# Optimization experiments

Measured on AMD Instinct MI355X. Metric: run time of the kernel, lower is better.

The kernel has to match this reference:

```python
import jax, jax.numpy as jnp
import numpy as np

K_F = 3          # propagation kernel
PAD_F = 1
NUM = K_F * K_F - 1   # 8 non-reference neighbors
IDX_REF = NUM // 2    # 4
PROP_TIME = 18
B, H, W = 4, 240, 1216


def _conv2d_same(x, w, b):
    # x: (B,Cin,H,W), w: (Cout,Cin,kh,kw)
    y = jax.lax.conv_general_dilated(x, w, (1, 1), 'SAME',
                                     dimension_numbers=('NCHW', 'OIHW', 'NCHW'))
    return y + b[None, :, None, None]


def _bilinear(img, y, x):
    # img: (B,H,W); y,x: (B,K,H,W) float sample coords. Zero outside bounds (DCN semantics).
    Bv, Hv, Wv = img.shape
    flat = img.reshape(Bv, -1)
    y0 = jnp.floor(y)
    x0 = jnp.floor(x)
    wy = y - y0
    wx = x - x0

    def g(yy, xx):
        valid = (yy >= 0) & (yy <= Hv - 1) & (xx >= 0) & (xx <= Wv - 1)
        yc = jnp.clip(yy, 0, Hv - 1).astype(jnp.int32)
        xc = jnp.clip(xx, 0, Wv - 1).astype(jnp.int32)
        idx = (yc * Wv + xc).reshape(Bv, -1)
        v = jnp.take_along_axis(flat, idx, axis=1).reshape(yy.shape)
        return jnp.where(valid, v, jnp.zeros((), img.dtype))

    return ((1 - wy) * (1 - wx) * g(y0, x0)
            + (1 - wy) * wx * g(y0, x0 + 1)
            + wy * (1 - wx) * g(y1 := y0 + 1, x0)
            + wy * wx * g(y1, x0 + 1))


def _deform_agg(feat, off, mask, k, pad):
    # Modulated deformable conv with w == 1, b == 0, ch_f == 1.
    # feat: (B,1,H,W); off: (B,K,2,H,W) (dy,dx); mask: (B,K,H,W)
    Bv, _, Hv, Wv = feat.shape
    kk = jnp.arange(k)
    by = (jnp.repeat(kk, k) - pad).astype(feat.dtype)  # kernel base dy, row-major
    bx = (jnp.tile(kk, k) - pad).astype(feat.dtype)    # kernel base dx
    gy = jnp.arange(Hv, dtype=feat.dtype)[None, None, :, None]
    gx = jnp.arange(Wv, dtype=feat.dtype)[None, None, None, :]
    y = gy + by[None, :, None, None] + off[:, :, 0]
    x = gx + bx[None, :, None, None] + off[:, :, 1]
    s = _bilinear(feat[:, 0], y, x)                    # (B,K,H,W)
    return jnp.sum(s * mask, axis=1, keepdims=True)


def setup_inputs() -> dict:
    key = jax.random.key(0)
    k1, k2, k3, k4, k5, k6 = jax.random.split(key, 6)
    feat_init = jax.random.uniform(k1, (B, 1, H, W), jnp.float32)
    guidance = jax.random.normal(k2, (B, 8, H, W), jnp.float32)
    confidence = jax.random.uniform(k3, (B, 1, H, W), jnp.float32)
    dep = jax.random.uniform(k4, (B, 1, H, W), jnp.float32)
    valid = (jax.random.uniform(k5, (B, 1, H, W), jnp.float32) < 0.05)
    feat_fix = dep * valid.astype(jnp.float32)
    w_oa = 0.1 * jax.random.normal(k6, (3 * NUM, 8, 3, 3), jnp.float32)
    b_oa = jnp.zeros((3 * NUM,), jnp.float32)
    aff_scale_const = jnp.full((1,), 0.5 * NUM, jnp.float32)  # gamma * num (TGASS)
    return {'feat_init': feat_init, 'guidance': guidance, 'confidence': confidence,
            'feat_fix': feat_fix, 'w_oa': w_oa, 'b_oa': b_oa,
            'aff_scale_const': aff_scale_const}


def reference(feat_init, guidance, confidence, feat_fix, w_oa, b_oa, aff_scale_const):
    Bv, _, Hv, Wv = guidance.shape
    oa = _conv2d_same(guidance, w_oa, b_oa)                 # (B,24,H,W)
    o1, o2, aff = oa[:, :NUM], oa[:, NUM:2 * NUM], oa[:, 2 * NUM:]
    # torch: cat((o1,o2),1).view(B,num,2,H,W) then insert zero ref offset at idx_ref
    off = jnp.concatenate([o1, o2], axis=1).reshape(Bv, NUM, 2, Hv, Wv)
    zeros = jnp.zeros((Bv, 1, 2, Hv, Wv), off.dtype)
    off = jnp.concatenate([off[:, :IDX_REF], zeros, off[:, IDX_REF:]], axis=1)  # (B,9,2,H,W)

    # TGASS affinity
    aff = jnp.tanh(aff) / (aff_scale_const + 1e-8)          # (B,8,H,W)

    # confidence-weighted affinity: 1x1 deform-sample of confidence at each neighbor offset
    nbr = jnp.array([0, 1, 2, 3, 5, 6, 7, 8])
    off_c = jax.lax.stop_gradient(off[:, nbr])              # (B,8,2,H,W), offsets detached
    gy = jnp.arange(Hv, dtype=aff.dtype)[None, None, :, None]
    gx = jnp.arange(Wv, dtype=aff.dtype)[None, None, None, :]
    conf_aff = _bilinear(confidence[:, 0], gy + off_c[:, :, 0], gx + off_c[:, :, 1])
    aff = aff * conf_aff

    s = jnp.sum(jnp.abs(aff), axis=1, keepdims=True) + 1e-4
    s = jnp.maximum(s, 1.0)                                 # TGASS clamp
    aff = aff / s
    aff_ref = 1.0 - jnp.sum(aff, axis=1, keepdims=True)
    aff9 = jnp.concatenate([aff[:, :IDX_REF], aff_ref, aff[:, IDX_REF:]], axis=1)  # (B,9,H,W)

    # preserve_input mask
    mask_fix = (jnp.sum((feat_fix > 0.0).astype(feat_fix.dtype), axis=1, keepdims=True) > 0.0)
    mask_fix = jax.lax.stop_gradient(mask_fix.astype(feat_fix.dtype))

    def step(feat, _):
        feat = (1.0 - mask_fix) * feat + mask_fix * feat_fix
        feat = _deform_agg(feat, off, aff9, K_F, PAD_F)
        return feat, None

    feat_result, _ = jax.lax.scan(step, feat_init, None, length=PROP_TIME)
    return feat_result, off.reshape(Bv, -1, Hv, Wv), aff9
```

## Files before the change

### kernel.cpp

```cpp
#include <hip/hip_runtime.h>
#include <hip/hip_bf16.h>

#define B_ 4
#define H_ 240
#define W_ 1216
#define HW_ (H_*W_)
#define N1_ (B_*HW_)
#define PT_ 18

#define PR_ 4
#define TROWS2 (PR_ + 10)
#define TCOLS 274

__device__ __forceinline__ bool probe_bf16(const void* scale_ptr) {
    return ((const unsigned short*)scale_ptr)[0] == 0x4080;
}

__device__ __forceinline__ float ldin(const void* p, int i, bool bf) {
    if (bf) {
        unsigned int u = (unsigned int)((const unsigned short*)p)[i];
        return __uint_as_float(u << 16);
    }
    return ((const float*)p)[i];
}

__device__ __forceinline__ void stout(void* p, int i, bool bf, float v) {
    if (bf) ((__hip_bfloat16*)p)[i] = __float2bfloat16(v);
    else    ((float*)p)[i] = v;
}

__global__ __launch_bounds__(256) void k_prep_w(const void* __restrict__ w_oa,
                                                const void* __restrict__ b_oa,
                                                const void* __restrict__ scale,
                                                float* __restrict__ wc) {
    bool bf = probe_bf16(scale);
    int i = blockIdx.x * 256 + threadIdx.x;
    if (i < 1728) wc[i] = ldin(w_oa, i, bf);
    if (i < 24)   wc[1728 + i] = ldin(b_oa, i, bf);
}

__global__ __launch_bounds__(256) void k_init(const void* __restrict__ finit,
                                              const void* __restrict__ ffix,
                                              const void* __restrict__ scale,
                                              float* __restrict__ featA) {
    bool bf = probe_bf16(scale);
    int p = blockIdx.x * 256 + threadIdx.x;
    if (p >= N1_) return;
    float fx = ldin(ffix, p, bf);
    featA[p] = (fx > 0.0f) ? fx : ldin(finit, p, bf);
}

__global__ __launch_bounds__(256) void k_conv(const void* __restrict__ guid,
                                              const void* __restrict__ conf,
                                              const void* __restrict__ scale,
                                              const float* __restrict__ wc,
                                              void* __restrict__ d_out,
                                              float* __restrict__ ws_off,
                                              float* __restrict__ ws_aff,
                                              int mode2) {
    bool bf = probe_bf16(scale);
    int p = blockIdx.x * 256 + threadIdx.x;
    if (p >= N1_) return;
    int b = p / HW_;
    int r = p - b * HW_;
    int h = r / W_;
    int w = r - h * W_;

    float g[8][9];
    #pragma unroll
    for (int t = 0; t < 9; ++t) {
        int hh = h + t / 3 - 1;
        int ww = w + t % 3 - 1;
        bool v = (hh >= 0) && (hh < H_) && (ww >= 0) && (ww < W_);
        int idx0 = hh * W_ + ww;
        #pragma unroll
        for (int ci = 0; ci < 8; ++ci)
            g[ci][t] = v ? ldin(guid, (b * 8 + ci) * HW_ + idx0, bf) : 0.0f;
    }

    float oa[24];
    #pragma unroll
    for (int co = 0; co < 24; ++co) {
        float a = wc[1728 + co];
        #pragma unroll
        for (int ci = 0; ci < 8; ++ci)
            #pragma unroll
            for (int t = 0; t < 9; ++t)
                a = fmaf(g[ci][t], wc[(co * 8 + ci) * 9 + t], a);
        oa[co] = a;
    }

    float scl = ldin(scale, 0, bf);
    float inv = 1.0f / (scl + 1e-8f);

    float aft[8];
    int cbase = b * HW_;
    #pragma unroll
    for (int t = 0; t < 8; ++t) {
        float a = tanhf(oa[16 + t]) * inv;
        float y = (float)h + oa[2 * t];
        float x = (float)w + oa[2 * t + 1];
        float y0f = floorf(y), x0f = floorf(x);
        int y0 = (int)y0f, x0 = (int)x0f;
        float wy = y - y0f, wx = x - x0f;
        int y0c = min(max(y0, 0), H_ - 1), y1c = min(max(y0 + 1, 0), H_ - 1);
        int x0c = min(max(x0, 0), W_ - 1), x1c = min(max(x0 + 1, 0), W_ - 1);
        bool vy0 = (y0 >= 0) && (y0 < H_), vy1 = (y0 >= -1) && (y0 < H_ - 1);
        bool vx0 = (x0 >= 0) && (x0 < W_), vx1 = (x0 >= -1) && (x0 < W_ - 1);
        float w00 = (1.0f - wy) * (1.0f - wx); w00 = (vy0 && vx0) ? w00 : 0.0f;
        float w01 = (1.0f - wy) * wx;          w01 = (vy0 && vx1) ? w01 : 0.0f;
        float w10 = wy * (1.0f - wx);          w10 = (vy1 && vx0) ? w10 : 0.0f;
        float w11 = wy * wx;                   w11 = (vy1 && vx1) ? w11 : 0.0f;
        float f00 = ldin(conf, cbase + y0c * W_ + x0c, bf);
        float f01 = ldin(conf, cbase + y0c * W_ + x1c, bf);
        float f10 = ldin(conf, cbase + y1c * W_ + x0c, bf);
        float f11 = ldin(conf, cbase + y1c * W_ + x1c, bf);
        float cv = w00 * f00 + w01 * f01 + w10 * f10 + w11 * f11;
        aft[t] = a * cv;
    }
    float s = 1e-4f;
    #pragma unroll
    for (int t = 0; t < 8; ++t) s += fabsf(aft[t]);
    s = fmaxf(s, 1.0f);
    float rs = 1.0f / s;
    float suma = 0.0f;
    #pragma unroll
    for (int t = 0; t < 8; ++t) { aft[t] *= rs; suma += aft[t]; }
    float aref = 1.0f - suma;

    #pragma unroll
    for (int t = 0; t < 8; ++t) {
        int n9 = t + (t >= 4 ? 1 : 0);
        stout(d_out, N1_ + (b * 18 + 2 * n9)     * HW_ + r, bf, oa[2 * t]);
        stout(d_out, N1_ + (b * 18 + 2 * n9 + 1) * HW_ + r, bf, oa[2 * t + 1]);
        stout(d_out, 19 * N1_ + (b * 9 + n9) * HW_ + r, bf, aft[t]);
    }
    stout(d_out, N1_ + (b * 18 + 8) * HW_ + r, bf, 0.0f);
    stout(d_out, N1_ + (b * 18 + 9) * HW_ + r, bf, 0.0f);
    stout(d_out, 19 * N1_ + (b * 9 + 4) * HW_ + r, bf, aref);

    if (mode2 && bf) {
        #pragma unroll
        for (int t = 0; t < 8; ++t) {
            ws_off[t * N1_ + p]       = oa[2 * t];
            ws_off[(8 + t) * N1_ + p] = oa[2 * t + 1];
            int n9 = t + (t >= 4 ? 1 : 0);
            ws_aff[n9 * N1_ + p] = aft[t];
        }
        ws_aff[4 * N1_ + p] = aref;
    }
}

__global__ __launch_bounds__(256) void k_prop(const float* __restrict__ src,
                                              float* __restrict__ dst,
                                              const float* __restrict__ ws_off,
                                              const float* __restrict__ ws_aff,
                                              const void* __restrict__ d_out_all,
                                              const void* __restrict__ ffix_in,
                                              const void* __restrict__ scale,
                                              void* __restrict__ d_out_feat,
                                              int last, int mode2) {
    __shared__ float tile[TROWS2][TCOLS];

    int tx = threadIdx.x;
    int bx = blockIdx.x;
    int h0 = blockIdx.y * PR_;
    int b  = blockIdx.z;
    int w  = bx * 256 + tx;
    bool active = (w < W_);
    bool bf = probe_bf16(scale);
    bool use_ws = (mode2 != 0) && bf;

    const float* sp = src + b * HW_;
    int row0 = h0 - 5;
    int col0 = bx * 256 - 8;

    for (int idx = tx; idx < TROWS2 * TCOLS; idx += 256) {
        int rr = idx / TCOLS;
        int cc = idx - rr * TCOLS;
        int gy = min(max(row0 + rr, 0), H_ - 1);
        int gx = min(max(col0 + cc, 0), W_ - 1);
        tile[rr][cc] = sp[gy * W_ + gx];
    }
    __syncthreads();
    if (!active) return;

    for (int ry = 0; ry < PR_; ++ry) {
        int h = h0 + ry;
        int r = h * W_ + w;
        int p = b * HW_ + r;

        float oy[8], ox[8], af[9];
        if (use_ws) {
            #pragma unroll
            for (int t = 0; t < 8; ++t) {
                oy[t] = ws_off[t * N1_ + p];
                ox[t] = ws_off[(8 + t) * N1_ + p];
            }
            #pragma unroll
            for (int n = 0; n < 9; ++n) af[n] = ws_aff[n * N1_ + p];
        } else {
            #pragma unroll
            for (int t = 0; t < 8; ++t) {
                int n9 = t + (t >= 4 ? 1 : 0);
                oy[t] = ldin(d_out_all, N1_ + (b * 18 + 2 * n9)     * HW_ + r, bf);
                ox[t] = ldin(d_out_all, N1_ + (b * 18 + 2 * n9 + 1) * HW_ + r, bf);
            }
            #pragma unroll
            for (int n = 0; n < 9; ++n)
                af[n] = ldin(d_out_all, 19 * N1_ + (b * 9 + n) * HW_ + r, bf);
        }

        float acc = af[4] * tile[5 + ry][tx + 8];

        #pragma unroll
        for (int t = 0; t < 8; ++t) {
            int n9 = t + (t >= 4 ? 1 : 0);
            float y = (float)(h + n9 / 3 - 1) + oy[t];
            float x = (float)(w + n9 % 3 - 1) + ox[t];
            float y0f = floorf(y), x0f = floorf(x);
            int y0 = (int)y0f, x0 = (int)x0f;
            float wy = y - y0f, wx = x - x0f;
            int y0c = min(max(y0, 0), H_ - 1), y1c = min(max(y0 + 1, 0), H_ - 1);
            int x0c = min(max(x0, 0), W_ - 1), x1c = min(max(x0 + 1, 0), W_ - 1);
            bool vy0 = (y0 >= 0) && (y0 < H_), vy1 = (y0 >= -1) && (y0 < H_ - 1);
            bool vx0 = (x0 >= 0) && (x0 < W_), vx1 = (x0 >= -1) && (x0 < W_ - 1);
            float w00 = (1.0f - wy) * (1.0f - wx); w00 = (vy0 && vx0) ? w00 : 0.0f;
            float w01 = (1.0f - wy) * wx;          w01 = (vy0 && vx1) ? w01 : 0.0f;
            float w10 = wy * (1.0f - wx);          w10 = (vy1 && vx0) ? w10 : 0.0f;
            float w11 = wy * wx;                   w11 = (vy1 && vx1) ? w11 : 0.0f;

            int sy0 = y0c - row0, sy1 = y1c - row0;
            int sx0 = x0c - col0, sx1 = x1c - col0;
            float f00, f01, f10, f11;
            if ((sy0 >= 0) && (sy1 <= TROWS2 - 1) && (sx0 >= 0) && (sx1 <= TCOLS - 1)) {
                f00 = tile[sy0][sx0];
                f01 = tile[sy0][sx1];
                f10 = tile[sy1][sx0];
                f11 = tile[sy1][sx1];
            } else {
                f00 = sp[y0c * W_ + x0c];
                f01 = sp[y0c * W_ + x1c];
                f10 = sp[y1c * W_ + x0c];
                f11 = sp[y1c * W_ + x1c];
            }
            float v = w00 * f00 + w01 * f01 + w10 * f10 + w11 * f11;
            acc = fmaf(af[n9], v, acc);
        }

        if (last) {
            stout(d_out_feat, p, bf, acc);
        } else {
            float fxv = ldin(ffix_in, p, bf);
            dst[p] = (fxv > 0.0f) ? fxv : acc;
        }
    }
}

extern "C" void kernel_launch(void* const* d_in, const int* in_sizes, int n_in,
                              void* d_out, int out_size, void* d_ws, size_t ws_size,
                              hipStream_t stream) {
    const void* feat_init  = d_in[0];
    const void* guidance   = d_in[1];
    const void* confidence = d_in[2];
    const void* feat_fix   = d_in[3];
    const void* w_oa       = d_in[4];
    const void* b_oa       = d_in[5];
    const void* scale      = d_in[6];

    float* wsf    = (float*)d_ws;
    float* featA  = wsf;
    float* featB  = wsf + N1_;
    float* wc     = wsf + 2 * (size_t)N1_;
    float* ws_off = wsf + 2 * (size_t)N1_ + 4096;
    float* ws_aff = ws_off + 16 * (size_t)N1_;

    size_t need2 = ((size_t)27 * N1_ + 4096) * sizeof(float);
    int mode2 = (ws_size >= need2) ? 1 : 0;

    int grid = (N1_ + 255) / 256;
    hipLaunchKernelGGL(k_prep_w, dim3(7), dim3(256), 0, stream, w_oa, b_oa, scale, wc);
    hipLaunchKernelGGL(k_init, dim3(grid), dim3(256), 0, stream,
                       feat_init, feat_fix, scale, featA);
    hipLaunchKernelGGL(k_conv, dim3(grid), dim3(256), 0, stream,
                       guidance, confidence, scale, wc, d_out, ws_off, ws_aff, mode2);

    float* a = featA;
    float* bbuf = featB;
    dim3 pgrid(5, H_ / PR_, B_);
    for (int it = 0; it < PT_; ++it) {
        int last = (it == PT_ - 1) ? 1 : 0;
        hipLaunchKernelGGL(k_prop, pgrid, dim3(256), 0, stream,
                           a, bbuf, ws_off, ws_aff, d_out, feat_fix, scale,
                           d_out, last, mode2);
        float* t = a; a = bbuf; bbuf = t;
    }
}
```

Baseline: 990.5 us.

## Replace per-step fixed-depth reload with bitmask, template dtype paths, restructure conv loop

The init kernel now builds a 64-bit ballot bitmask of fixed (sparse-depth) pixels and writes the initial feature into both ping-pong buffers. Each propagation step then skips storing fixed pixels instead of reloading feat_fix every iteration, which cuts global reads in the 18 prop launches. Kernels are templated on bf16/fp32 so the dtype branch is resolved once per launch. The conv loop is reordered to load one input channel at a time, which lowers register pressure. Correctness relies on fixed pixels already holding their value in both buffers, and the grid size now assumes N1 is divisible by 256.

```diff
diff --git a/kernel.cpp b/kernel.cpp
--- a/kernel.cpp
+++ b/kernel.cpp
@@ -16,16 +16,18 @@
     return ((const unsigned short*)scale_ptr)[0] == 0x4080;
 }
 
-__device__ __forceinline__ float ldin(const void* p, int i, bool bf) {
-    if (bf) {
+template<bool BF>
+__device__ __forceinline__ float ldT(const void* p, int i) {
+    if (BF) {
         unsigned int u = (unsigned int)((const unsigned short*)p)[i];
         return __uint_as_float(u << 16);
     }
     return ((const float*)p)[i];
 }
 
-__device__ __forceinline__ void stout(void* p, int i, bool bf, float v) {
-    if (bf) ((__hip_bfloat16*)p)[i] = __float2bfloat16(v);
+template<bool BF>
+__device__ __forceinline__ void stT(void* p, int i, float v) {
+    if (BF) ((__hip_bfloat16*)p)[i] = __float2bfloat16(v);
     else    ((float*)p)[i] = v;
 }
 
@@ -35,62 +37,71 @@
                                                 float* __restrict__ wc) {
     bool bf = probe_bf16(scale);
     int i = blockIdx.x * 256 + threadIdx.x;
-    if (i < 1728) wc[i] = ldin(w_oa, i, bf);
-    if (i < 24)   wc[1728 + i] = ldin(b_oa, i, bf);
+    if (i < 1728) wc[i] = bf ? ldT<true>(w_oa, i) : ldT<false>(w_oa, i);
+    if (i < 24)   wc[1728 + i] = bf ? ldT<true>(b_oa, i) : ldT<false>(b_oa, i);
 }
 
 __global__ __launch_bounds__(256) void k_init(const void* __restrict__ finit,
                                               const void* __restrict__ ffix,
                                               const void* __restrict__ scale,
-                                              float* __restrict__ featA) {
+                                              float* __restrict__ featA,
+                                              float* __restrict__ featB,
+                                              unsigned long long* __restrict__ mask64) {
     bool bf = probe_bf16(scale);
     int p = blockIdx.x * 256 + threadIdx.x;
-    if (p >= N1_) return;
-    float fx = ldin(ffix, p, bf);
-    featA[p] = (fx > 0.0f) ? fx : ldin(finit, p, bf);
-}
-
-__global__ __launch_bounds__(256) void k_conv(const void* __restrict__ guid,
-                                              const void* __restrict__ conf,
-                                              const void* __restrict__ scale,
-                                              const float* __restrict__ wc,
-                                              void* __restrict__ d_out,
-                                              float* __restrict__ ws_off,
-                                              float* __restrict__ ws_aff,
-                                              int mode2) {
-    bool bf = probe_bf16(scale);
+    float fx = bf ? ldT<true>(ffix, p)  : ldT<false>(ffix, p);
+    float fi = bf ? ldT<true>(finit, p) : ldT<false>(finit, p);
+    bool fixed = fx > 0.0f;
+    float v = fixed ? fx : fi;
+    featA[p] = v;
+    featB[p] = v;
+    unsigned long long bal = __ballot(fixed);
+    if ((threadIdx.x & 63) == 0) mask64[p >> 6] = bal;
+}
+
+template<bool BF>
+__device__ __forceinline__ void conv_body(const void* __restrict__ guid,
+                                          const void* __restrict__ conf,
+                                          const void* __restrict__ scale,
+                                          const float* __restrict__ wc,
+                                          void* __restrict__ d_out,
+                                          float* __restrict__ ws_off,
+                                          float* __restrict__ ws_aff,
+                                          int mode2) {
     int p = blockIdx.x * 256 + threadIdx.x;
-    if (p >= N1_) return;
     int b = p / HW_;
     int r = p - b * HW_;
     int h = r / W_;
     int w = r - h * W_;
 
-    float g[8][9];
+    int idx0[9]; bool vld[9];
     #pragma unroll
     for (int t = 0; t < 9; ++t) {
         int hh = h + t / 3 - 1;
         int ww = w + t % 3 - 1;
-        bool v = (hh >= 0) && (hh < H_) && (ww >= 0) && (ww < W_);
-        int idx0 = hh * W_ + ww;
+        vld[t] = (hh >= 0) && (hh < H_) && (ww >= 0) && (ww < W_);
+        idx0[t] = hh * W_ + ww;
+    }
+
+    float oa[24];
+    #pragma unroll
+    for (int co = 0; co < 24; ++co) oa[co] = wc[1728 + co];
+
+    #pragma unroll
+    for (int ci = 0; ci < 8; ++ci) {
+        int cb = (b * 8 + ci) * HW_;
+        float gv[9];
         #pragma unroll
-        for (int ci = 0; ci < 8; ++ci)
-            g[ci][t] = v ? ldin(guid, (b * 8 + ci) * HW_ + idx0, bf) : 0.0f;
-    }
-
-    float oa[24];
-    #pragma unroll
-    for (int co = 0; co < 24; ++co) {
-        float a = wc[1728 + co];
+        for (int t = 0; t < 9; ++t)
+            gv[t] = vld[t] ? ldT<BF>(guid, cb + idx0[t]) : 0.0f;
         #pragma unroll
-        for (int ci = 0; ci < 8; ++ci)
+        for (int co = 0; co < 24; ++co)
             #pragma unroll
             for (int t = 0; t < 9; ++t)
-                a = fmaf(g[ci][t], wc[(co * 8 + ci) * 9 + t], a);
-        oa[co] = a;
-    }
-
-    float scl = ldin(scale, 0, bf);
+                oa[co] = fmaf(gv[t], wc[(co * 8 + ci) * 9 + t], oa[co]);
+    }
+
+    float scl = ldT<BF>(scale, 0);
     float inv = 1.0f / (scl + 1e-8f);
 
     float aft[8];
@@ -111,10 +122,10 @@
         float w01 = (1.0f - wy) * wx;          w01 = (vy0 && vx1) ? w01 : 0.0f;
         float w10 = wy * (1.0f - wx);          w10 = (vy1 && vx0) ? w10 : 0.0f;
         float w11 = wy * wx;                   w11 = (vy1 && vx1) ? w11 : 0.0f;
-        float f00 = ldin(conf, cbase + y0c * W_ + x0c, bf);
-        float f01 = ldin(conf, cbase + y0c * W_ + x1c, bf);
-        float f10 = ldin(conf, cbase + y1c * W_ + x0c, bf);
-        float f11 = ldin(conf, cbase + y1c * W_ + x1c, bf);
+        float f00 = ldT<BF>(conf, cbase + y0c * W_ + x0c);
+        float f01 = ldT<BF>(conf, cbase + y0c * W_ + x1c);
+        float f10 = ldT<BF>(conf, cbase + y1c * W_ + x0c);
+        float f11 = ldT<BF>(conf, cbase + y1c * W_ + x1c);
         float cv = w00 * f00 + w01 * f01 + w10 * f10 + w11 * f11;
         aft[t] = a * cv;
     }
@@ -131,15 +142,15 @@
     #pragma unroll
     for (int t = 0; t < 8; ++t) {
         int n9 = t + (t >= 4 ? 1 : 0);
-        stout(d_out, N1_ + (b * 18 + 2 * n9)     * HW_ + r, bf, oa[2 * t]);
-        stout(d_out, N1_ + (b * 18 + 2 * n9 + 1) * HW_ + r, bf, oa[2 * t + 1]);
-        stout(d_out, 19 * N1_ + (b * 9 + n9) * HW_ + r, bf, aft[t]);
-    }
-    stout(d_out, N1_ + (b * 18 + 8) * HW_ + r, bf, 0.0f);
-    stout(d_out, N1_ + (b * 18 + 9) * HW_ + r, bf, 0.0f);
-    stout(d_out, 19 * N1_ + (b * 9 + 4) * HW_ + r, bf, aref);
-
-    if (mode2 && bf) {
+        stT<BF>(d_out, N1_ + (b * 18 + 2 * n9)     * HW_ + r, oa[2 * t]);
+        stT<BF>(d_out, N1_ + (b * 18 + 2 * n9 + 1) * HW_ + r, oa[2 * t + 1]);
+        stT<BF>(d_out, 19 * N1_ + (b * 9 + n9) * HW_ + r, aft[t]);
+    }
+    stT<BF>(d_out, N1_ + (b * 18 + 8) * HW_ + r, 0.0f);
+    stT<BF>(d_out, N1_ + (b * 18 + 9) * HW_ + r, 0.0f);
+    stT<BF>(d_out, 19 * N1_ + (b * 9 + 4) * HW_ + r, aref);
+
+    if (BF && mode2) {
         #pragma unroll
         for (int t = 0; t < 8; ++t) {
             ws_off[t * N1_ + p]       = oa[2 * t];
@@ -151,25 +162,37 @@
     }
 }
 
-__global__ __launch_bounds__(256) void k_prop(const float* __restrict__ src,
-                                              float* __restrict__ dst,
-                                              const float* __restrict__ ws_off,
-                                              const float* __restrict__ ws_aff,
-                                              const void* __restrict__ d_out_all,
-                                              const void* __restrict__ ffix_in,
+__global__ __launch_bounds__(256) void k_conv(const void* __restrict__ guid,
+                                              const void* __restrict__ conf,
                                               const void* __restrict__ scale,
-                                              void* __restrict__ d_out_feat,
-                                              int last, int mode2) {
-    __shared__ float tile[TROWS2][TCOLS];
-
+                                              const float* __restrict__ wc,
+                                              void* __restrict__ d_out,
+                                              float* __restrict__ ws_off,
+                                              float* __restrict__ ws_aff,
+                                              int mode2) {
+    if (probe_bf16(scale))
+        conv_body<true>(guid, conf, scale, wc, d_out, ws_off, ws_aff, mode2);
+    else
+        conv_body<false>(guid, conf, scale, wc, d_out, ws_off, ws_aff, mode2);
+}
+
+template<bool BF>
+__device__ __forceinline__ void prop_body(float (*tile)[TCOLS],
+                                          const float* __restrict__ src,
+                                          float* __restrict__ dst,
+                                          const float* __restrict__ ws_off,
+                                          const float* __restrict__ ws_aff,
+                                          const void* __restrict__ d_out_all,
+                                          const unsigned long long* __restrict__ mask64,
+                                          void* __restrict__ d_out_feat,
+                                          int last, int mode2) {
     int tx = threadIdx.x;
     int bx = blockIdx.x;
     int h0 = blockIdx.y * PR_;
     int b  = blockIdx.z;
     int w  = bx * 256 + tx;
     bool active = (w < W_);
-    bool bf = probe_bf16(scale);
-    bool use_ws = (mode2 != 0) && bf;
+    bool use_ws = BF && (mode2 != 0);
 
     const float* sp = src + b * HW_;
     int row0 = h0 - 5;
@@ -203,12 +226,12 @@
             #pragma unroll
             for (int t = 0; t < 8; ++t) {
                 int n9 = t + (t >= 4 ? 1 : 0);
-                oy[t] = ldin(d_out_all, N1_ + (b * 18 + 2 * n9)     * HW_ + r, bf);
-                ox[t] = ldin(d_out_all, N1_ + (b * 18 + 2 * n9 + 1) * HW_ + r, bf);
+                oy[t] = ldT<BF>(d_out_all, N1_ + (b * 18 + 2 * n9)     * HW_ + r);
+                ox[t] = ldT<BF>(d_out_all, N1_ + (b * 18 + 2 * n9 + 1) * HW_ + r);
             }
             #pragma unroll
             for (int n = 0; n < 9; ++n)
-                af[n] = ldin(d_out_all, 19 * N1_ + (b * 9 + n) * HW_ + r, bf);
+                af[n] = ldT<BF>(d_out_all, 19 * N1_ + (b * 9 + n) * HW_ + r);
         }
 
         float acc = af[4] * tile[5 + ry][tx + 8];
@@ -249,12 +272,31 @@
         }
 
         if (last) {
-            stout(d_out_feat, p, bf, acc);
+            stT<BF>(d_out_feat, p, acc);
         } else {
-            float fxv = ldin(ffix_in, p, bf);
-            dst[p] = (fxv > 0.0f) ? fxv : acc;
+            unsigned long long bal = mask64[p >> 6];
+            bool fixed = (bal >> (p & 63)) & 1ull;
+            if (!fixed) dst[p] = acc;
         }
     }
+}
+
+__global__ __launch_bounds__(256) void k_prop(const float* __restrict__ src,
+                                              float* __restrict__ dst,
+                                              const float* __restrict__ ws_off,
+                                              const float* __restrict__ ws_aff,
+                                              const void* __restrict__ d_out_all,
+                                              const unsigned long long* __restrict__ mask64,
+                                              const void* __restrict__ scale,
+                                              void* __restrict__ d_out_feat,
+                                              int last, int mode2) {
+    __shared__ float tile[TROWS2][TCOLS];
+    if (probe_bf16(scale))
+        prop_body<true>(tile, src, dst, ws_off, ws_aff, d_out_all, mask64,
+                        d_out_feat, last, mode2);
+    else
+        prop_body<false>(tile, src, dst, ws_off, ws_aff, d_out_all, mask64,
+                         d_out_feat, last, mode2);
 }
 
 extern "C" void kernel_launch(void* const* d_in, const int* in_sizes, int n_in,
@@ -272,16 +314,18 @@
     float* featA  = wsf;
     float* featB  = wsf + N1_;
     float* wc     = wsf + 2 * (size_t)N1_;
-    float* ws_off = wsf + 2 * (size_t)N1_ + 4096;
+    unsigned long long* mask64 =
+        (unsigned long long*)(wsf + 2 * (size_t)N1_ + 2048);
+    float* ws_off = wsf + 2 * (size_t)N1_ + 2048 + 36480;
     float* ws_aff = ws_off + 16 * (size_t)N1_;
 
-    size_t need2 = ((size_t)27 * N1_ + 4096) * sizeof(float);
+    size_t need2 = ((size_t)27 * N1_ + 2048 + 36480) * sizeof(float);
     int mode2 = (ws_size >= need2) ? 1 : 0;
 
-    int grid = (N1_ + 255) / 256;
+    int grid = N1_ / 256;
     hipLaunchKernelGGL(k_prep_w, dim3(7), dim3(256), 0, stream, w_oa, b_oa, scale, wc);
     hipLaunchKernelGGL(k_init, dim3(grid), dim3(256), 0, stream,
-                       feat_init, feat_fix, scale, featA);
+                       feat_init, feat_fix, scale, featA, featB, mask64);
     hipLaunchKernelGGL(k_conv, dim3(grid), dim3(256), 0, stream,
                        guidance, confidence, scale, wc, d_out, ws_off, ws_aff, mode2);
 
@@ -291,7 +335,7 @@
     for (int it = 0; it < PT_; ++it) {
         int last = (it == PT_ - 1) ? 1 : 0;
         hipLaunchKernelGGL(k_prop, pgrid, dim3(256), 0, stream,
-                           a, bbuf, ws_off, ws_aff, d_out, feat_fix, scale,
+                           a, bbuf, ws_off, ws_aff, d_out, mask64, scale,
                            d_out, last, mode2);
         float* t = a; a = bbuf; bbuf = t;
     }
```

After: 987.8 us. About the same (-0.3%).

## Precompute fixed-pixel bitmask, skip fixed writes, template prop on dtype, halve rows per block

Applied to the files above, without the earlier changes.

k_init now writes the initial feature into both ping-pong buffers and builds a 64-bit ballot bitmask of fixed (sparse-depth) pixels. The propagation kernel reads one mask word instead of reloading feat_fix every iteration, and it skips stores for fixed pixels because those values stay valid in both buffers. The propagation body is templated on the bf16/fp32 dtype so the per-load branch is gone, and PR_ drops from 4 to 2, which doubles the block count but raises the halo overhead per tile. The grid size no longer rounds up and the bounds check is removed, which only holds because N1_ divides evenly by 256.

```diff
diff --git a/kernel.cpp b/kernel.cpp
--- a/kernel.cpp
+++ b/kernel.cpp
@@ -8,7 +8,7 @@
 #define N1_ (B_*HW_)
 #define PT_ 18
 
-#define PR_ 4
+#define PR_ 2
 #define TROWS2 (PR_ + 10)
 #define TCOLS 274
 
@@ -26,6 +26,21 @@
 
 __device__ __forceinline__ void stout(void* p, int i, bool bf, float v) {
     if (bf) ((__hip_bfloat16*)p)[i] = __float2bfloat16(v);
+    else    ((float*)p)[i] = v;
+}
+
+template<bool BF>
+__device__ __forceinline__ float ldT(const void* p, int i) {
+    if (BF) {
+        unsigned int u = (unsigned int)((const unsigned short*)p)[i];
+        return __uint_as_float(u << 16);
+    }
+    return ((const float*)p)[i];
+}
+
+template<bool BF>
+__device__ __forceinline__ void stT(void* p, int i, float v) {
+    if (BF) ((__hip_bfloat16*)p)[i] = __float2bfloat16(v);
     else    ((float*)p)[i] = v;
 }
 
@@ -42,12 +57,19 @@
 __global__ __launch_bounds__(256) void k_init(const void* __restrict__ finit,
                                               const void* __restrict__ ffix,
                                               const void* __restrict__ scale,
-                                              float* __restrict__ featA) {
+                                              float* __restrict__ featA,
+                                              float* __restrict__ featB,
+                                              unsigned long long* __restrict__ mask64) {
     bool bf = probe_bf16(scale);
     int p = blockIdx.x * 256 + threadIdx.x;
-    if (p >= N1_) return;
     float fx = ldin(ffix, p, bf);
-    featA[p] = (fx > 0.0f) ? fx : ldin(finit, p, bf);
+    float fi = ldin(finit, p, bf);
+    bool fixed = fx > 0.0f;
+    float v = fixed ? fx : fi;
+    featA[p] = v;
+    featB[p] = v;
+    unsigned long long bal = __ballot(fixed);
+    if ((threadIdx.x & 63) == 0) mask64[p >> 6] = bal;
 }
 
 __global__ __launch_bounds__(256) void k_conv(const void* __restrict__ guid,
@@ -151,25 +173,23 @@
     }
 }
 
-__global__ __launch_bounds__(256) void k_prop(const float* __restrict__ src,
-                                              float* __restrict__ dst,
-                                              const float* __restrict__ ws_off,
-                                              const float* __restrict__ ws_aff,
-                                              const void* __restrict__ d_out_all,
-                                              const void* __restrict__ ffix_in,
-                                              const void* __restrict__ scale,
-                                              void* __restrict__ d_out_feat,
-                                              int last, int mode2) {
-    __shared__ float tile[TROWS2][TCOLS];
-
+template<bool BF>
+__device__ __forceinline__ void prop_body(float (*tile)[TCOLS],
+                                          const float* __restrict__ src,
+                                          float* __restrict__ dst,
+                                          const float* __restrict__ ws_off,
+                                          const float* __restrict__ ws_aff,
+                                          const void* __restrict__ d_out_all,
+                                          const unsigned long long* __restrict__ mask64,
+                                          void* __restrict__ d_out_feat,
+                                          int last, int mode2) {
     int tx = threadIdx.x;
     int bx = blockIdx.x;
     int h0 = blockIdx.y * PR_;
     int b  = blockIdx.z;
     int w  = bx * 256 + tx;
     bool active = (w < W_);
-    bool bf = probe_bf16(scale);
-    bool use_ws = (mode2 != 0) && bf;
+    bool use_ws = BF && (mode2 != 0);
 
     const float* sp = src + b * HW_;
     int row0 = h0 - 5;
@@ -203,12 +223,12 @@
             #pragma unroll
             for (int t = 0; t < 8; ++t) {
                 int n9 = t + (t >= 4 ? 1 : 0);
-                oy[t] = ldin(d_out_all, N1_ + (b * 18 + 2 * n9)     * HW_ + r, bf);
-                ox[t] = ldin(d_out_all, N1_ + (b * 18 + 2 * n9 + 1) * HW_ + r, bf);
+                oy[t] = ldT<BF>(d_out_all, N1_ + (b * 18 + 2 * n9)     * HW_ + r);
+                ox[t] = ldT<BF>(d_out_all, N1_ + (b * 18 + 2 * n9 + 1) * HW_ + r);
             }
             #pragma unroll
             for (int n = 0; n < 9; ++n)
-                af[n] = ldin(d_out_all, 19 * N1_ + (b * 9 + n) * HW_ + r, bf);
+                af[n] = ldT<BF>(d_out_all, 19 * N1_ + (b * 9 + n) * HW_ + r);
         }
 
         float acc = af[4] * tile[5 + ry][tx + 8];
@@ -249,12 +269,31 @@
         }
 
         if (last) {
-            stout(d_out_feat, p, bf, acc);
+            stT<BF>(d_out_feat, p, acc);
         } else {
-            float fxv = ldin(ffix_in, p, bf);
-            dst[p] = (fxv > 0.0f) ? fxv : acc;
+            unsigned long long bal = mask64[p >> 6];
+            bool fixed = (bal >> (p & 63)) & 1ull;
+            if (!fixed) dst[p] = acc;
         }
     }
+}
+
+__global__ __launch_bounds__(256) void k_prop(const float* __restrict__ src,
+                                              float* __restrict__ dst,
+                                              const float* __restrict__ ws_off,
+                                              const float* __restrict__ ws_aff,
+                                              const void* __restrict__ d_out_all,
+                                              const unsigned long long* __restrict__ mask64,
+                                              const void* __restrict__ scale,
+                                              void* __restrict__ d_out_feat,
+                                              int last, int mode2) {
+    __shared__ float tile[TROWS2][TCOLS];
+    if (probe_bf16(scale))
+        prop_body<true>(tile, src, dst, ws_off, ws_aff, d_out_all, mask64,
+                        d_out_feat, last, mode2);
+    else
+        prop_body<false>(tile, src, dst, ws_off, ws_aff, d_out_all, mask64,
+                         d_out_feat, last, mode2);
 }
 
 extern "C" void kernel_launch(void* const* d_in, const int* in_sizes, int n_in,
@@ -272,16 +311,18 @@
     float* featA  = wsf;
     float* featB  = wsf + N1_;
     float* wc     = wsf + 2 * (size_t)N1_;
-    float* ws_off = wsf + 2 * (size_t)N1_ + 4096;
+    unsigned long long* mask64 =
+        (unsigned long long*)(wsf + 2 * (size_t)N1_ + 2048);
+    float* ws_off = wsf + 2 * (size_t)N1_ + 2048 + 36480;
     float* ws_aff = ws_off + 16 * (size_t)N1_;
 
-    size_t need2 = ((size_t)27 * N1_ + 4096) * sizeof(float);
+    size_t need2 = ((size_t)27 * N1_ + 2048 + 36480) * sizeof(float);
     int mode2 = (ws_size >= need2) ? 1 : 0;
 
-    int grid = (N1_ + 255) / 256;
+    int grid = N1_ / 256;
     hipLaunchKernelGGL(k_prep_w, dim3(7), dim3(256), 0, stream, w_oa, b_oa, scale, wc);
     hipLaunchKernelGGL(k_init, dim3(grid), dim3(256), 0, stream,
-                       feat_init, feat_fix, scale, featA);
+                       feat_init, feat_fix, scale, featA, featB, mask64);
     hipLaunchKernelGGL(k_conv, dim3(grid), dim3(256), 0, stream,
                        guidance, confidence, scale, wc, d_out, ws_off, ws_aff, mode2);
 
@@ -291,7 +332,7 @@
     for (int it = 0; it < PT_; ++it) {
         int last = (it == PT_ - 1) ? 1 : 0;
         hipLaunchKernelGGL(k_prop, pgrid, dim3(256), 0, stream,
-                           a, bbuf, ws_off, ws_aff, d_out, feat_fix, scale,
+                           a, bbuf, ws_off, ws_aff, d_out, mask64, scale,
                            d_out, last, mode2);
         float* t = a; a = bbuf; bbuf = t;
     }
```

After: 955.9 us. -3.5%, faster.
